# Performance work log

Measured on AMD Instinct MI355X. Metric: run time of the kernel, lower is better.

## Reference

```python
import jax, jax.numpy as jnp
import numpy as np


def setup_inputs() -> dict:
    key = jax.random.key(0)
    ks = jax.random.split(key, 9)
    B, T, F_IN = 128, 2048, 32
    R, H, F_OUT = 256, 256, 32
    s = lambda k, shape, fan: jax.random.normal(k, shape, dtype=jnp.float32) * (1.0 / np.sqrt(fan))
    return {
        "input_seq": jax.random.normal(ks[0], (B, T, F_IN), dtype=jnp.float32),
        "enc_W": s(ks[1], (R, F_IN), F_IN),
        "enc_b": s(ks[2], (R,), F_IN),
        "W_ih": s(ks[3], (4 * H, R), H),
        "W_hh": s(ks[4], (4 * H, H), H),
        "b_ih": s(ks[5], (4 * H,), H),
        "b_hh": s(ks[6], (4 * H,), H),
        "dec_W": s(ks[7], (F_OUT, H), H),
        "dec_b": s(ks[8], (F_OUT,), H),
        "future_n": 64,
    }


def reference(input_seq, enc_W, enc_b, W_ih, W_hh, b_ih, b_hh, dec_W, dec_b, future_n):
    # Faithful to source: `state` is never updated inside the loop, so every
    # timestep applies the LSTMCell to the SAME initial state (eval: zeros).
    B, T, _ = input_seq.shape
    H = W_hh.shape[1]
    h0 = jnp.zeros((B, H), dtype=input_seq.dtype)
    c0 = jnp.zeros((B, H), dtype=input_seq.dtype)

    encoded = jnp.einsum('btf,rf->btr', input_seq, enc_W) + enc_b  # [B,T,R]
    # future steps all reuse the last encoded timestep
    last = jnp.broadcast_to(encoded[:, -1:, :], (B, future_n, encoded.shape[-1]))
    enc_full = jnp.concatenate([encoded, last], axis=1)  # [B, T+future_n, R]

    # LSTMCell gates (PyTorch order: i, f, g, o); state contribution is constant.
    state_gates = h0 @ W_hh.T + b_hh  # [B, 4H] (zeros state -> just b_hh)
    gates = jnp.einsum('btr,gr->btg', enc_full, W_ih) + b_ih + state_gates[:, None, :]
    i, f, g, o = jnp.split(gates, 4, axis=-1)
    c = jax.nn.sigmoid(f) * c0[:, None, :] + jax.nn.sigmoid(i) * jnp.tanh(g)
    h = jax.nn.sigmoid(o) * jnp.tanh(c)  # [B, T+future_n, H]

    return jnp.einsum('bth,oh->bto', h, dec_W) + dec_b
```

## Files before the change

kernel.cpp:

```cpp
#include <hip/hip_runtime.h>


typedef _Float16 f16x8 __attribute__((ext_vector_type(8)));
typedef _Float16 f16x4 __attribute__((ext_vector_type(4)));
typedef float    f32x4 __attribute__((ext_vector_type(4)));
typedef __fp16   h16x2 __attribute__((ext_vector_type(2)));

#define T_IN 2048
#define TT   2112
#define FIN  32
#define FOUT 32

#define WS_FB_OFF   49152
#define WS_DECW_OFF 52224

union PkU { h16x2 h; unsigned u; };

__global__ __launch_bounds__(256) void prep2(
    const float* __restrict__ enc_W, const float* __restrict__ enc_b,
    const float* __restrict__ W_ih, const float* __restrict__ b_ih,
    const float* __restrict__ b_hh, const float* __restrict__ dec_W,
    _Float16* __restrict__ Mb, float* __restrict__ fb, _Float16* __restrict__ decWb) {
    const int blk = blockIdx.x;
    const int tid = threadIdx.x;
    if (blk < 768) {
        const int gg = blk, sg = gg + (gg >= 256 ? 256 : 0);
        const float* wr = W_ih + (size_t)sg * 256;
        const int f = tid & 31, r8 = tid >> 5;
        float acc = 0.f;
#pragma unroll
        for (int k = 0; k < 32; ++k) {
            int r = r8 * 32 + k;
            acc = fmaf(wr[r], enc_W[r * 32 + f], acc);
        }
        __shared__ float red[256];
        __shared__ float redb[256];
        __shared__ float red2[32];
        red[tid]  = acc;
        redb[tid] = wr[tid] * enc_b[tid];
        __syncthreads();
        if (tid < 32) {
            float s = 0.f;
#pragma unroll
            for (int k = 0; k < 8; ++k) s += red[k * 32 + tid];
            Mb[gg * 32 + tid] = (_Float16)s;
        } else if (tid >= 128 && tid < 160) {
            int t2 = tid - 128;
            float s2 = 0.f;
#pragma unroll
            for (int k = 0; k < 8; ++k) s2 += redb[t2 * 8 + k];
            red2[t2] = s2;
        }
        __syncthreads();
        if (tid == 0) {
            float t = b_ih[sg] + b_hh[sg];
#pragma unroll
            for (int k = 0; k < 32; ++k) t += red2[k];
            fb[gg] = t;
        }
    } else {
        int i = (blk - 768) * 1024 + tid * 4;
        f32x4 v = *(const f32x4*)(dec_W + i);
        f16x4 o;
#pragma unroll
        for (int j = 0; j < 4; ++j) o[j] = (_Float16)v[j];
        *(f16x4*)(decWb + i) = o;
    }
}

__global__ __launch_bounds__(256) void lstm_main(
    const float* __restrict__ in, const _Float16* __restrict__ Mb,
    const float* __restrict__ fb, const _Float16* __restrict__ decWb,
    const float* __restrict__ dec_b, float* __restrict__ out) {
    __shared__ _Float16 hbuf[4][2][16 * 40];

    const int lane = threadIdx.x & 63;
    const int w    = threadIdx.x >> 6;
    const int l16  = lane & 15;
    const int q    = lane >> 4;
    const int wave = blockIdx.x * 4 + w;
    const int rowbase = wave * 32;
    const int b  = rowbase / TT;
    const int t0 = rowbase - b * TT;

    f16x8 bfr[2];
#pragma unroll
    for (int s = 0; s < 2; ++s) {
        int t  = t0 + s * 16 + l16;
        int tr = t < T_IN ? t : (T_IN - 1);
        const float* p = in + ((size_t)(b * T_IN + tr)) * FIN + q * 8;
        f32x4 u0 = *(const f32x4*)(p);
        f32x4 u1 = *(const f32x4*)(p + 4);
        f16x8 v;
#pragma unroll
        for (int j = 0; j < 4; ++j) { v[j] = (_Float16)u0[j]; v[4 + j] = (_Float16)u1[j]; }
        bfr[s] = v;
    }

    f32x4 dacc[2][2];
#pragma unroll
    for (int ot = 0; ot < 2; ++ot) {
        f32x4 db = *(const f32x4*)(dec_b + ot * 16 + q * 4);
        dacc[0][ot] = db; dacc[1][ot] = db;
    }

    for (int hc = 0; hc < 8; ++hc) {
        const int hb = hc * 32;
        f16x8 afr[3][2];
        f32x4 fbv[3][2];
#pragma unroll
        for (int gt = 0; gt < 3; ++gt)
#pragma unroll
            for (int X = 0; X < 2; ++X) {
                int grow = gt * 256 + hb + X * 16;
                afr[gt][X] = *(const f16x8*)(Mb + (size_t)(grow + l16) * 32 + q * 8);
                fbv[gt][X] = *(const f32x4*)(fb + grow + q * 4);
            }
        f16x8 a2[2];
#pragma unroll
        for (int ot = 0; ot < 2; ++ot)
            a2[ot] = *(const f16x8*)(decWb + (size_t)(ot * 16 + l16) * 256 + hb + q * 8);

#pragma unroll
        for (int s = 0; s < 2; ++s) {
            f32x4 gi[2], gg[2], go[2];
#pragma unroll
            for (int X = 0; X < 2; ++X) {
                gi[X] = __builtin_amdgcn_mfma_f32_16x16x32_f16(afr[0][X], bfr[s], fbv[0][X], 0, 0, 0);
                gg[X] = __builtin_amdgcn_mfma_f32_16x16x32_f16(afr[1][X], bfr[s], fbv[1][X], 0, 0, 0);
                go[X] = __builtin_amdgcn_mfma_f32_16x16x32_f16(afr[2][X], bfr[s], fbv[2][X], 0, 0, 0);
            }
            _Float16* hp = &hbuf[w][s][0];
#pragma unroll
            for (int X = 0; X < 2; ++X) {
                float hv[4];
#pragma unroll
                for (int r = 0; r < 4; ++r) {
                    float iv = gi[X][r], gv = gg[X][r], ov = go[X][r];
                    float U  = __builtin_amdgcn_exp2f(-1.4426950408889634f * iv);
                    float gc = fminf(gv, 30.f);
                    float E  = __builtin_amdgcn_exp2f(2.8853900817779268f * gc);
                    float c  = (E - 1.0f) * __builtin_amdgcn_rcpf((1.0f + U) * (1.0f + E));
                    float z  = c * c;
                    float P  = fmaf(z, fmaf(z, fmaf(z, fmaf(z, -5.70498872745e-3f,
                                    2.06390887954e-2f), -5.37397155531e-2f),
                                    1.33314422036e-1f), -3.33332819422e-1f);
                    float tc = fmaf(c * z, P, c);
                    float Uo = __builtin_amdgcn_exp2f(-1.4426950408889634f * ov);
                    float so = __builtin_amdgcn_rcpf(1.0f + Uo);
                    hv[r] = so * tc;
                }
                PkU p0, p1;
                p0.h = __builtin_amdgcn_cvt_pkrtz(hv[0], hv[1]);
                p1.h = __builtin_amdgcn_cvt_pkrtz(hv[2], hv[3]);
                uint2 wv = { p0.u, p1.u };
                *(uint2*)(hp + l16 * 40 + X * 16 + q * 4) = wv;
            }
            asm volatile("s_waitcnt lgkmcnt(0)" ::: "memory");
            f16x8 b2 = *(const f16x8*)(hp + l16 * 40 + q * 8);
#pragma unroll
            for (int ot = 0; ot < 2; ++ot)
                dacc[s][ot] = __builtin_amdgcn_mfma_f32_16x16x32_f16(a2[ot], b2, dacc[s][ot], 0, 0, 0);
        }
    }

#pragma unroll
    for (int s = 0; s < 2; ++s) {
        int t = t0 + s * 16 + l16;
        size_t ro = ((size_t)(b * TT + t)) * FOUT;
#pragma unroll
        for (int ot = 0; ot < 2; ++ot)
            *(f32x4*)(out + ro + ot * 16 + q * 4) = dacc[s][ot];
    }
}

extern "C" void kernel_launch(void* const* d_in, const int* in_sizes, int n_in,
                              void* d_out, int out_size, void* d_ws, size_t ws_size,
                              hipStream_t stream) {
    const float* input = (const float*)d_in[0];
    const float* enc_W = (const float*)d_in[1];
    const float* enc_b = (const float*)d_in[2];
    const float* W_ih  = (const float*)d_in[3];
    const float* b_ih  = (const float*)d_in[5];
    const float* b_hh  = (const float*)d_in[6];
    const float* dec_W = (const float*)d_in[7];
    const float* dec_b = (const float*)d_in[8];

    _Float16* Mb    = (_Float16*)d_ws;
    float*    fb    = (float*)((char*)d_ws + WS_FB_OFF);
    _Float16* decWb = (_Float16*)((char*)d_ws + WS_DECW_OFF);
    float*    out   = (float*)d_out;

    prep2<<<776, 256, 0, stream>>>(enc_W, enc_b, W_ih, b_ih, b_hh, dec_W, Mb, fb, decWb);
    lstm_main<<<2112, 256, 0, stream>>>(input, Mb, fb, decWb, dec_b, out);
}
```

Baseline: 169.2 us.

## Process four row tiles per wave and batch the decoder MFMAs after gates

Each wave now handles 64 timestep rows (four 16-row slices) instead of 32, so per-chunk weight and bias fragments loaded from global memory are reused across twice as many rows, and the grid is halved. The gate computation for all slices runs first, followed by a single LDS wait and then the decoder MFMAs, replacing the per-slice wait. The input fp32-to-fp16 conversion uses packed conversion intrinsics, and launch bounds request two blocks per CU. The cost is higher register pressure and fewer waves, which could reduce latency hiding.

```diff
diff --git a/kernel.cpp b/kernel.cpp
--- a/kernel.cpp
+++ b/kernel.cpp
@@ -10,6 +10,7 @@
 #define TT   2112
 #define FIN  32
 #define FOUT 32
+#define NS   4
 
 #define WS_FB_OFF   49152
 #define WS_DECW_OFF 52224
@@ -68,40 +69,45 @@
     }
 }
 
-__global__ __launch_bounds__(256) void lstm_main(
+__global__ __launch_bounds__(256, 2) void lstm_main(
     const float* __restrict__ in, const _Float16* __restrict__ Mb,
     const float* __restrict__ fb, const _Float16* __restrict__ decWb,
     const float* __restrict__ dec_b, float* __restrict__ out) {
-    __shared__ _Float16 hbuf[4][2][16 * 40];
+    __shared__ _Float16 hbuf[4][NS][16 * 40];
 
     const int lane = threadIdx.x & 63;
     const int w    = threadIdx.x >> 6;
     const int l16  = lane & 15;
     const int q    = lane >> 4;
     const int wave = blockIdx.x * 4 + w;
-    const int rowbase = wave * 32;
+    const int rowbase = wave * (16 * NS);
     const int b  = rowbase / TT;
     const int t0 = rowbase - b * TT;
 
-    f16x8 bfr[2];
-#pragma unroll
-    for (int s = 0; s < 2; ++s) {
+    f16x8 bfr[NS];
+#pragma unroll
+    for (int s = 0; s < NS; ++s) {
         int t  = t0 + s * 16 + l16;
         int tr = t < T_IN ? t : (T_IN - 1);
         const float* p = in + ((size_t)(b * T_IN + tr)) * FIN + q * 8;
         f32x4 u0 = *(const f32x4*)(p);
         f32x4 u1 = *(const f32x4*)(p + 4);
-        f16x8 v;
-#pragma unroll
-        for (int j = 0; j < 4; ++j) { v[j] = (_Float16)u0[j]; v[4 + j] = (_Float16)u1[j]; }
-        bfr[s] = v;
-    }
-
-    f32x4 dacc[2][2];
+        PkU c0, c1, c2, c3;
+        c0.h = __builtin_amdgcn_cvt_pkrtz(u0[0], u0[1]);
+        c1.h = __builtin_amdgcn_cvt_pkrtz(u0[2], u0[3]);
+        c2.h = __builtin_amdgcn_cvt_pkrtz(u1[0], u1[1]);
+        c3.h = __builtin_amdgcn_cvt_pkrtz(u1[2], u1[3]);
+        union { f16x8 v; uint4 u; } pk;
+        pk.u = (uint4){ c0.u, c1.u, c2.u, c3.u };
+        bfr[s] = pk.v;
+    }
+
+    f32x4 dacc[NS][2];
 #pragma unroll
     for (int ot = 0; ot < 2; ++ot) {
         f32x4 db = *(const f32x4*)(dec_b + ot * 16 + q * 4);
-        dacc[0][ot] = db; dacc[1][ot] = db;
+#pragma unroll
+        for (int s = 0; s < NS; ++s) dacc[s][ot] = db;
     }
 
     for (int hc = 0; hc < 8; ++hc) {
@@ -122,7 +128,7 @@
             a2[ot] = *(const f16x8*)(decWb + (size_t)(ot * 16 + l16) * 256 + hb + q * 8);
 
 #pragma unroll
-        for (int s = 0; s < 2; ++s) {
+        for (int s = 0; s < NS; ++s) {
             f32x4 gi[2], gg[2], go[2];
 #pragma unroll
             for (int X = 0; X < 2; ++X) {
@@ -156,7 +162,13 @@
                 uint2 wv = { p0.u, p1.u };
                 *(uint2*)(hp + l16 * 40 + X * 16 + q * 4) = wv;
             }
-            asm volatile("s_waitcnt lgkmcnt(0)" ::: "memory");
+        }
+
+        asm volatile("s_waitcnt lgkmcnt(0)" ::: "memory");
+
+#pragma unroll
+        for (int s = 0; s < NS; ++s) {
+            const _Float16* hp = &hbuf[w][s][0];
             f16x8 b2 = *(const f16x8*)(hp + l16 * 40 + q * 8);
 #pragma unroll
             for (int ot = 0; ot < 2; ++ot)
@@ -165,7 +177,7 @@
     }
 
 #pragma unroll
-    for (int s = 0; s < 2; ++s) {
+    for (int s = 0; s < NS; ++s) {
         int t = t0 + s * 16 + l16;
         size_t ro = ((size_t)(b * TT + t)) * FOUT;
 #pragma unroll
@@ -192,5 +204,5 @@
     float*    out   = (float*)d_out;
 
     prep2<<<776, 256, 0, stream>>>(enc_W, enc_b, W_ih, b_ih, b_hh, dec_W, Mb, fb, decWb);
-    lstm_main<<<2112, 256, 0, stream>>>(input, Mb, fb, decWb, dec_b, out);
+    lstm_main<<<1056, 256, 0, stream>>>(input, Mb, fb, decWb, dec_b, out);
 }
```

After: 186.7 us. 10.3% more time.

## Compute LSTM gate activations with packed fp16 rational approximations

Applied to the files above, without the earlier changes.

The gate epilogue no longer uses scalar fp32 exp2/rcp per element. It now converts the gate pre-activations to packed half pairs and evaluates sigmoid and tanh through one clamped rational Padé tanh, sharing a single reciprocal across the three gates, followed by a short odd polynomial for tanh(c). The prep kernel folds the x/8 (sigmoid) and x/4 (tanh) argument scalings into the fused weights and biases, so the kernel needs no extra multiply. This cuts transcendental and VALU cost in the compute-bound epilogue, at the price of lower accuracy: half precision, a clamped saturation range, and an approximate final tanh.

```diff
diff --git a/kernel.cpp b/kernel.cpp
--- a/kernel.cpp
+++ b/kernel.cpp
@@ -4,7 +4,8 @@
 typedef _Float16 f16x8 __attribute__((ext_vector_type(8)));
 typedef _Float16 f16x4 __attribute__((ext_vector_type(4)));
 typedef float    f32x4 __attribute__((ext_vector_type(4)));
-typedef __fp16   h16x2 __attribute__((ext_vector_type(2)));
+typedef _Float16 hx2   __attribute__((ext_vector_type(2)));
+typedef __fp16   pk16x2 __attribute__((ext_vector_type(2)));
 
 #define T_IN 2048
 #define TT   2112
@@ -14,7 +15,14 @@
 #define WS_FB_OFF   49152
 #define WS_DECW_OFF 52224
 
-union PkU { h16x2 h; unsigned u; };
+union PkCast { pk16x2 p; hx2 h; unsigned u; };
+
+__device__ __forceinline__ hx2 pk2(float a, float b) {
+    PkCast c; c.p = __builtin_amdgcn_cvt_pkrtz(a, b); return c.h;
+}
+__device__ __forceinline__ hx2 splat(float v) {
+    _Float16 h = (_Float16)v; return (hx2){h, h};
+}
 
 __global__ __launch_bounds__(256) void prep2(
     const float* __restrict__ enc_W, const float* __restrict__ enc_b,
@@ -25,6 +33,7 @@
     const int tid = threadIdx.x;
     if (blk < 768) {
         const int gg = blk, sg = gg + (gg >= 256 ? 256 : 0);
+        const float scale = (gg >= 256 && gg < 512) ? 0.25f : 0.125f;
         const float* wr = W_ih + (size_t)sg * 256;
         const int f = tid & 31, r8 = tid >> 5;
         float acc = 0.f;
@@ -43,7 +52,7 @@
             float s = 0.f;
 #pragma unroll
             for (int k = 0; k < 8; ++k) s += red[k * 32 + tid];
-            Mb[gg * 32 + tid] = (_Float16)s;
+            Mb[gg * 32 + tid] = (_Float16)(s * scale);
         } else if (tid >= 128 && tid < 160) {
             int t2 = tid - 128;
             float s2 = 0.f;
@@ -56,7 +65,7 @@
             float t = b_ih[sg] + b_hh[sg];
 #pragma unroll
             for (int k = 0; k < 32; ++k) t += red2[k];
-            fb[gg] = t;
+            fb[gg] = t * scale;
         }
     } else {
         int i = (blk - 768) * 1024 + tid * 4;
@@ -83,6 +92,12 @@
     const int b  = rowbase / TT;
     const int t0 = rowbase - b * TT;
 
+    const hx2 C0 = splat(4.0f),      C1 = splat(7.757576f), C2 = splat(2.068687f);
+    const hx2 D1 = splat(7.272727f), D2 = splat(5.171717f), D3 = splat(0.394036f);
+    const hx2 ONE = splat(1.0f), NEG1 = splat(-1.0f), H05 = splat(0.5f);
+    const hx2 T0 = splat(0.99980f), T1 = splat(-0.32806f),
+              T2 = splat(0.11306f), T3 = splat(-0.02344f);
+
     f16x8 bfr[2];
 #pragma unroll
     for (int s = 0; s < 2; ++s) {
@@ -91,10 +106,10 @@
         const float* p = in + ((size_t)(b * T_IN + tr)) * FIN + q * 8;
         f32x4 u0 = *(const f32x4*)(p);
         f32x4 u1 = *(const f32x4*)(p + 4);
-        f16x8 v;
-#pragma unroll
-        for (int j = 0; j < 4; ++j) { v[j] = (_Float16)u0[j]; v[4 + j] = (_Float16)u1[j]; }
-        bfr[s] = v;
+        union { hx2 h[4]; f16x8 v; } pk;
+        pk.h[0] = pk2(u0[0], u0[1]); pk.h[1] = pk2(u0[2], u0[3]);
+        pk.h[2] = pk2(u1[0], u1[1]); pk.h[3] = pk2(u1[2], u1[3]);
+        bfr[s] = pk.v;
     }
 
     f32x4 dacc[2][2];
@@ -133,28 +148,39 @@
             _Float16* hp = &hbuf[w][s][0];
 #pragma unroll
             for (int X = 0; X < 2; ++X) {
-                float hv[4];
-#pragma unroll
-                for (int r = 0; r < 4; ++r) {
-                    float iv = gi[X][r], gv = gg[X][r], ov = go[X][r];
-                    float U  = __builtin_amdgcn_exp2f(-1.4426950408889634f * iv);
-                    float gc = fminf(gv, 30.f);
-                    float E  = __builtin_amdgcn_exp2f(2.8853900817779268f * gc);
-                    float c  = (E - 1.0f) * __builtin_amdgcn_rcpf((1.0f + U) * (1.0f + E));
-                    float z  = c * c;
-                    float P  = fmaf(z, fmaf(z, fmaf(z, fmaf(z, -5.70498872745e-3f,
-                                    2.06390887954e-2f), -5.37397155531e-2f),
-                                    1.33314422036e-1f), -3.33332819422e-1f);
-                    float tc = fmaf(c * z, P, c);
-                    float Uo = __builtin_amdgcn_exp2f(-1.4426950408889634f * ov);
-                    float so = __builtin_amdgcn_rcpf(1.0f + Uo);
-                    hv[r] = so * tc;
+                hx2 hpair[2];
+#pragma unroll
+                for (int p = 0; p < 2; ++p) {
+                    hx2 ui = pk2(gi[X][2 * p], gi[X][2 * p + 1]);
+                    hx2 ug = pk2(gg[X][2 * p], gg[X][2 * p + 1]);
+                    hx2 uo = pk2(go[X][2 * p], go[X][2 * p + 1]);
+                    ui = __builtin_elementwise_max(__builtin_elementwise_min(ui, ONE), NEG1);
+                    ug = __builtin_elementwise_max(__builtin_elementwise_min(ug, ONE), NEG1);
+                    uo = __builtin_elementwise_max(__builtin_elementwise_min(uo, ONE), NEG1);
+                    hx2 wi = ui * ui, wg = ug * ug, wo = uo * uo;
+                    hx2 ni = ui * (wi * (wi * C2 + C1) + C0);
+                    hx2 ng = ug * (wg * (wg * C2 + C1) + C0);
+                    hx2 no = uo * (wo * (wo * C2 + C1) + C0);
+                    hx2 di = wi * (wi * (wi * D3 + D2) + D1) + ONE;
+                    hx2 dg = wg * (wg * (wg * D3 + D2) + D1) + ONE;
+                    hx2 dd = wo * (wo * (wo * D3 + D2) + D1) + ONE;
+                    hx2 pig = di * dg;
+                    hx2 Dp  = pig * dd;
+                    hx2 R   = pk2(__builtin_amdgcn_rcpf((float)Dp.x),
+                                  __builtin_amdgcn_rcpf((float)Dp.y));
+                    hx2 ti = ni * ((dg * dd) * R);
+                    hx2 tg = ng * ((di * dd) * R);
+                    hx2 to = no * (pig * R);
+                    hx2 si = ti * H05 + H05;
+                    hx2 so = to * H05 + H05;
+                    hx2 c  = si * tg;
+                    hx2 z  = c * c;
+                    hx2 P  = z * (z * (z * T3 + T2) + T1) + T0;
+                    hpair[p] = so * (c * P);
                 }
-                PkU p0, p1;
-                p0.h = __builtin_amdgcn_cvt_pkrtz(hv[0], hv[1]);
-                p1.h = __builtin_amdgcn_cvt_pkrtz(hv[2], hv[3]);
-                uint2 wv = { p0.u, p1.u };
-                *(uint2*)(hp + l16 * 40 + X * 16 + q * 4) = wv;
+                union { hx2 h[2]; uint2 u; } hw;
+                hw.h[0] = hpair[0]; hw.h[1] = hpair[1];
+                *(uint2*)(hp + l16 * 40 + X * 16 + q * 4) = hw.u;
             }
             asm volatile("s_waitcnt lgkmcnt(0)" ::: "memory");
             f16x8 b2 = *(const f16x8*)(hp + l16 * 40 + q * 8);
```

Result: no change. 170.1 us (+0.5%).
